# Performance work log

Hardware: AMD Instinct MI355X
Metric: run time of the kernel (lower is better)

Reference implementation:

```python
import jax, jax.numpy as jnp
import numpy as np

N_NODES = 50000
N_EDGES = 400000
IN_C, HID, EDGE_D = 128, 256, 32
NUM_LAYERS = 3

def _gnblock(x, src, dst, edge_attr, ew, eb, nw, nb):
    # edge message MLP: relu(W [x_src, x_dst, e] + b)  -> [E, HID]
    m = jax.nn.relu(jnp.concatenate([x[src], x[dst], edge_attr], axis=-1) @ ew + eb)
    # mean aggregation by destination node
    agg = jax.ops.segment_sum(m, dst, num_segments=N_NODES)
    deg = jax.ops.segment_sum(jnp.ones((m.shape[0],), m.dtype), dst, num_segments=N_NODES)
    agg = agg / jnp.maximum(deg, 1.0)[:, None]
    # node update MLP: relu(W [x, agg] + b) -> [N, HID]
    return jax.nn.relu(jnp.concatenate([x, agg], axis=-1) @ nw + nb)

def setup_inputs() -> dict:
    key = jax.random.key(0)
    ks = jax.random.split(key, 12)
    s = 0.05  # keep activations sane
    return {
        'x': jax.random.normal(ks[0], (N_NODES, IN_C), jnp.float32),
        'edge_index': jax.random.randint(ks[1], (2, N_EDGES), 0, N_NODES, jnp.int32),
        'edge_attr': jax.random.normal(ks[2], (N_EDGES, EDGE_D), jnp.float32),
        'e0_w': jax.random.normal(ks[3], (2 * IN_C + EDGE_D, HID), jnp.float32) * s,
        'e0_b': jnp.zeros((HID,), jnp.float32),
        'n0_w': jax.random.normal(ks[4], (IN_C + HID, HID), jnp.float32) * s,
        'n0_b': jnp.zeros((HID,), jnp.float32),
        'e_w': jax.random.normal(ks[5], (NUM_LAYERS - 1, 2 * HID + EDGE_D, HID), jnp.float32) * s,
        'e_b': jnp.zeros((NUM_LAYERS - 1, HID), jnp.float32),
        'n_w': jax.random.normal(ks[6], (NUM_LAYERS - 1, 2 * HID, HID), jnp.float32) * s,
        'n_b': jnp.zeros((NUM_LAYERS - 1, HID), jnp.float32),
        'h1_w': jax.random.normal(ks[7], (HID, HID), jnp.float32) * s,
        'h1_b': jnp.zeros((HID,), jnp.float32),
        'h2_w': jax.random.normal(ks[8], (HID, 1), jnp.float32) * s,
        'h2_b': jnp.zeros((1,), jnp.float32),
    }

def reference(x, edge_index, edge_attr, e0_w, e0_b, n0_w, n0_b,
              e_w, e_b, n_w, n_b, h1_w, h1_b, h2_w, h2_b):
    src, dst = edge_index[0], edge_index[1]
    h = _gnblock(x, src, dst, edge_attr, e0_w, e0_b, n0_w, n0_b)
    for i in range(NUM_LAYERS - 1):
        h = _gnblock(h, src, dst, edge_attr, e_w[i], e_b[i], n_w[i], n_b[i])
    # MLP head -> per-node logit [N, 1]
    h = jax.nn.relu(h @ h1_w + h1_b)
    return h @ h2_w + h2_b
```

## Files before the change

kernel.cpp:

```cpp
#include <hip/hip_runtime.h>
#include <hip/hip_bf16.h>
#include <hip/hip_fp16.h>

#define NN 50000
#define NE 400000
#define NBLK 196
#define PST 544

typedef unsigned short u16;
typedef unsigned int u32;
typedef __attribute__((ext_vector_type(8))) short short8;
typedef __attribute__((ext_vector_type(4))) float f32x4;
typedef __attribute__((ext_vector_type(4))) unsigned short u16x4;
typedef __attribute__((ext_vector_type(2))) _Float16 h2;
typedef __attribute__((ext_vector_type(16))) unsigned int u32x16;

typedef __attribute__((address_space(1))) const void as1_void;
typedef __attribute__((address_space(3))) void as3_void;

static __device__ __forceinline__ float bf2f(u16 u) {
    return __uint_as_float(((u32)u) << 16);
}
static __device__ __forceinline__ float bf2f_lo(u32 u) {
    return __uint_as_float(u << 16);
}
static __device__ __forceinline__ float bf2f_hi(u32 u) {
    return __uint_as_float(u & 0xffff0000u);
}
static __device__ __forceinline__ u16 f2bf(float f) {
    u32 x = __float_as_uint(f);
    x += 0x7fffu + ((x >> 16) & 1u);
    return (u16)(x >> 16);
}
static __device__ __forceinline__ u32 packbf2(float a, float b) {
    return ((u32)f2bf(b) << 16) | (u32)f2bf(a);
}
static __device__ __forceinline__ u32 packh2(float a, float b) {
    return ((u32)__half_as_ushort(__float2half(b)) << 16) |
           (u32)__half_as_ushort(__float2half(a));
}

static __device__ __forceinline__ void gload_lds16(const u16* g, u16* l) {
    __builtin_amdgcn_global_load_lds((as1_void*)g, (as3_void*)l, 16, 0, 0);
}

__global__ __launch_bounds__(256) void gemm_bt(
    const u16* __restrict__ A, int lda,
    const u16* __restrict__ Bt,
    u16* __restrict__ C, int ldc,
    int M, int K,
    const float* __restrict__ bias,
    int relu)
{
    __shared__ u16 As[128 * 32];
    __shared__ u16 Bs[128 * 32];

    const int t = threadIdx.x;
    const int w = t >> 6;
    const int lane = t & 63;
    const int quad = lane >> 4;
    const int l15 = lane & 15;
    const int tile_m = blockIdx.x * 128;
    const int tile_n = blockIdx.y * 128;
    const int wm = (w >> 1) * 64;
    const int wn = (w & 1) * 64;

    f32x4 acc[4][4];
#pragma unroll
    for (int r = 0; r < 4; ++r)
#pragma unroll
        for (int c = 0; c < 4; ++c)
            acc[r][c] = (f32x4){0.f, 0.f, 0.f, 0.f};

    int ar0 = tile_m + (t >> 2);      if (ar0 > M - 1) ar0 = M - 1;
    int ar1 = tile_m + 64 + (t >> 2); if (ar1 > M - 1) ar1 = M - 1;
    const int br0 = tile_n + (t >> 2);
    const int br1 = tile_n + 64 + (t >> 2);
    const int koff = (t & 3) * 8;

    u16* lAs0 = As + w * 512;
    u16* lAs1 = As + 2048 + w * 512;
    u16* lBs0 = Bs + w * 512;
    u16* lBs1 = Bs + 2048 + w * 512;

    const u16* Arow0 = A + (size_t)ar0 * lda + koff;
    const u16* Arow1 = A + (size_t)ar1 * lda + koff;
    const u16* Brow0 = Bt + (size_t)br0 * K + koff;
    const u16* Brow1 = Bt + (size_t)br1 * K + koff;

    for (int k0 = 0; k0 < K; k0 += 32) {
        gload_lds16(Arow0 + k0, lAs0);
        gload_lds16(Arow1 + k0, lAs1);
        gload_lds16(Brow0 + k0, lBs0);
        gload_lds16(Brow1 + k0, lBs1);
        __syncthreads();

        short8 af[4], bfr[4];
#pragma unroll
        for (int r = 0; r < 4; ++r)
            af[r] = *(const short8*)&As[(wm + r * 16 + l15) * 32 + quad * 8];
#pragma unroll
        for (int c = 0; c < 4; ++c)
            bfr[c] = *(const short8*)&Bs[(wn + c * 16 + l15) * 32 + quad * 8];
#pragma unroll
        for (int r = 0; r < 4; ++r)
#pragma unroll
            for (int c = 0; c < 4; ++c)
                acc[r][c] = __builtin_amdgcn_mfma_f32_16x16x32_bf16(af[r], bfr[c], acc[r][c], 0, 0, 0);
        __syncthreads();
    }

#pragma unroll
    for (int r = 0; r < 4; ++r) {
#pragma unroll
        for (int c = 0; c < 4; ++c) {
            const int coln = tile_n + wn + c * 16 + l15;
            const float bv = bias ? bias[coln] : 0.0f;
#pragma unroll
            for (int i = 0; i < 4; ++i) {
                const int row = tile_m + wm + r * 16 + quad * 4 + i;
                if (row < M) {
                    float v = acc[r][c][i] + bv;
                    if (relu) v = fmaxf(v, 0.f);
                    C[(size_t)row * ldc + coln] = f2bf(v);
                }
            }
        }
    }
}

__global__ __launch_bounds__(256) void edge_agg_fused(
    const u16* __restrict__ P,
    const u32* __restrict__ eattr_p32,
    const u32* __restrict__ WePk,
    const int* __restrict__ row_start,
    const int* __restrict__ src_perm,
    const float* __restrict__ inv_deg,
    u16* __restrict__ aggZ)
{
    __shared__ u32 Wlds[4096];

    const int t = threadIdx.x;
    {
        const u16* Wg = (const u16*)WePk;
        u16* Wl = (u16*)Wlds;
        const int wv = t >> 6;
        const int ln = t & 63;
#pragma unroll
        for (int r = 0; r < 4; ++r)
            gload_lds16(Wg + r * 2048 + wv * 512 + ln * 8,
                        Wl + r * 2048 + wv * 512);
    }
    __syncthreads();

    const int wid = (int)((blockIdx.x * 256 + t) >> 6);
    const int node = wid >> 1;
    const int half = wid & 1;
    const int lane = t & 63;
    const int coff = half * 128 + lane * 2;
    if (node >= NN) return;

    const u32 pdu = *(const u32*)(P + (size_t)node * PST + 256 + coff);
    const float pb0 = bf2f_lo(pdu);
    const float pb1 = bf2f_hi(pdu);

    float acc0 = 0.f, acc1 = 0.f;
    const int s0r = row_start[node], s1r = row_start[node + 1];

    if (s1r > s0r) {
        const int jlast = s1r - 1;
        const unsigned long long ebase =
            (unsigned long long)(uintptr_t)eattr_p32;

#define PSLD(ps, jj) do {                                                 \
        int js_ = __builtin_amdgcn_readfirstlane(                         \
            ((jj) < jlast) ? (jj) : jlast);                               \
        int ss_ = src_perm[js_];                                          \
        ps = *(const u32*)(P + (size_t)ss_ * PST + coff);                 \
    } while (0)

        u32 psA, psB;
        PSLD(psA, s0r);
        PSLD(psB, s0r + 1);

        for (int j = s0r; j < s1r; j += 2) {
            const u32 offA = (u32)__builtin_amdgcn_readfirstlane(j) << 6;
            const u32 offB = (u32)__builtin_amdgcn_readfirstlane(
                (j + 1 < jlast) ? j + 1 : jlast) << 6;
            u32x16 ea, eb;
            asm volatile("s_load_dwordx16 %0, %2, %3\n\t"
                         "s_load_dwordx16 %1, %2, %4"
                         : "=s"(ea), "=s"(eb)
                         : "s"(ebase), "s"(offA), "s"(offB));

            u32 psC, psD;
            PSLD(psC, j + 2);
            PSLD(psD, j + 3);

            asm volatile("s_waitcnt lgkmcnt(0)" ::: "memory");
            __builtin_amdgcn_sched_barrier(0);

            float q0A = pb0, q1A = pb1, q0B = pb0, q1B = pb1;
#define KP(idx)                                                           \
            {                                                             \
                uint2 wk = *(const uint2*)(Wlds + idx * 256 + coff);      \
                asm("v_dot2_f32_f16 %0, %4, %6, %0\n\t"                   \
                    "v_dot2_f32_f16 %1, %4, %7, %1\n\t"                   \
                    "v_dot2_f32_f16 %2, %5, %6, %2\n\t"                   \
                    "v_dot2_f32_f16 %3, %5, %7, %3"                       \
                    : "+v"(q0A), "+v"(q1A), "+v"(q0B), "+v"(q1B)          \
                    : "s"(ea[idx]), "s"(eb[idx]),                         \
                      "v"(wk.x), "v"(wk.y));                              \
            }
            KP(0)  KP(1)  KP(2)  KP(3)
            KP(4)  KP(5)  KP(6)  KP(7)
            KP(8)  KP(9)  KP(10) KP(11)
            KP(12) KP(13) KP(14) KP(15)
#undef KP

            q0A += bf2f_lo(psA);
            q1A += bf2f_hi(psA);
            acc0 += fmaxf(q0A, 0.f);
            acc1 += fmaxf(q1A, 0.f);

            q0B += bf2f_lo(psB);
            q1B += bf2f_hi(psB);
            const float m_ = (j + 1 < s1r) ? 1.0f : 0.0f;
            acc0 = fmaf(m_, fmaxf(q0B, 0.f), acc0);
            acc1 = fmaf(m_, fmaxf(q1B, 0.f), acc1);

            psA = psC;
            psB = psD;
        }
#undef PSLD
    }

    const float idg = inv_deg[node];
    *(u32*)(aggZ + (size_t)node * 512 + coff) = packbf2(acc0 * idg, acc1 * idg);
}

__global__ __launch_bounds__(256) void head_out(
    const u16* __restrict__ h4Z,
    const float* __restrict__ h2w,
    const float* __restrict__ h2b,
    float* __restrict__ out)
{
    const int node = (int)((blockIdx.x * 256 + threadIdx.x) >> 6);
    const int lane = threadIdx.x & 63;
    if (node >= NN) return;
    const int col = lane * 4;
    u16x4 hv = *(const u16x4*)(h4Z + (size_t)node * 512 + col);
    float4 wv = *(const float4*)(h2w + col);
    float s = bf2f(hv[0]) * wv.x + bf2f(hv[1]) * wv.y +
              bf2f(hv[2]) * wv.z + bf2f(hv[3]) * wv.w;
    for (int off = 32; off > 0; off >>= 1)
        s += __shfl_down(s, off, 64);
    if (lane == 0) out[node] = s + h2b[0];
}

__global__ void zero_int(int* p, int n) {
    int i = blockIdx.x * 256 + threadIdx.x;
    if (i < n) p[i] = 0;
}

__global__ void hist_k(const int* __restrict__ ei, int* __restrict__ deg) {
    int e = blockIdx.x * 256 + threadIdx.x;
    if (e < NE) atomicAdd(&deg[ei[NE + e]], 1);
}

__global__ __launch_bounds__(256) void block_sum_k(const int* __restrict__ deg,
                                                   int* __restrict__ bsum) {
    __shared__ int sm[4];
    const int i = blockIdx.x * 256 + threadIdx.x;
    int v = (i < NN) ? deg[i] : 0;
    for (int off = 32; off > 0; off >>= 1)
        v += __shfl_down(v, off, 64);
    const int lane = threadIdx.x & 63;
    const int w = threadIdx.x >> 6;
    if (lane == 0) sm[w] = v;
    __syncthreads();
    if (threadIdx.x == 0)
        bsum[blockIdx.x] = sm[0] + sm[1] + sm[2] + sm[3];
}

__global__ __launch_bounds__(256) void scan_block_k(const int* __restrict__ bsum,
                                                    int* __restrict__ boff,
                                                    int* __restrict__ row_start) {
    __shared__ int sm[256];
    const int tid = threadIdx.x;
    int v = (tid < NBLK) ? bsum[tid] : 0;
    sm[tid] = v;
    __syncthreads();
    for (int o = 1; o < 256; o <<= 1) {
        int tv = (tid >= o) ? sm[tid - o] : 0;
        __syncthreads();
        sm[tid] += tv;
        __syncthreads();
    }
    if (tid < NBLK) boff[tid] = sm[tid] - v;
    if (tid == NBLK - 1) row_start[NN] = sm[tid];
}

__global__ __launch_bounds__(256) void writeback_k(const int* __restrict__ deg,
                                                   const int* __restrict__ boff,
                                                   int* __restrict__ row_start,
                                                   int* __restrict__ cursor,
                                                   float* __restrict__ inv_deg) {
    __shared__ int sm[256];
    const int tid = threadIdx.x;
    const int i = blockIdx.x * 256 + tid;
    int v = (i < NN) ? deg[i] : 0;
    sm[tid] = v;
    __syncthreads();
    for (int o = 1; o < 256; o <<= 1) {
        int tv = (tid >= o) ? sm[tid - o] : 0;
        __syncthreads();
        sm[tid] += tv;
        __syncthreads();
    }
    if (i < NN) {
        const int rs = boff[blockIdx.x] + sm[tid] - v;
        row_start[i] = rs;
        cursor[i]    = rs;
        inv_deg[i]   = 1.0f / fmaxf((float)v, 1.0f);
    }
}

__global__ void scatter_k(const int* __restrict__ ei, const float* __restrict__ eattr,
                          int* __restrict__ cursor, int* __restrict__ src_perm,
                          u32* __restrict__ eattr_p32) {
    int e = blockIdx.x * 256 + threadIdx.x;
    if (e >= NE) return;
    int s = ei[e], d = ei[NE + e];
    int pos = atomicAdd(&cursor[d], 1);
    src_perm[pos] = s;
    const float* sr = eattr + (size_t)e * 32;
    u32 pk[16];
#pragma unroll
    for (int j = 0; j < 16; ++j)
        pk[j] = packh2(sr[2 * j], sr[2 * j + 1]);
    uint4* dr = (uint4*)(eattr_p32 + (size_t)pos * 16);
    dr[0] = (uint4){pk[0], pk[1], pk[2], pk[3]};
    dr[1] = (uint4){pk[4], pk[5], pk[6], pk[7]};
    dr[2] = (uint4){pk[8], pk[9], pk[10], pk[11]};
    dr[3] = (uint4){pk[12], pk[13], pk[14], pk[15]};
}

__global__ void bias_build(const float* __restrict__ e0b,
                           const float* __restrict__ eb1,
                           const float* __restrict__ eb2,
                           float* __restrict__ dst) {
    int i = blockIdx.x * 256 + threadIdx.x;
    if (i >= 1536) return;
    int l = i >> 9, c = i & 511;
    const float* s = (l == 0) ? e0b : (l == 1) ? eb1 : eb2;
    dst[i] = (c < 256) ? 0.f : s[c - 256];
}

struct TJob { const float* src; u16* dst; int K; int ksh; int tr; int dstride; };
struct TJobs { TJob j[16]; };

__global__ void transpose_k(TJobs jobs) {
    TJob jb = jobs.j[blockIdx.y];
    int idx = blockIdx.x * 256 + threadIdx.x;
    if (idx >= (jb.K << 8)) return;
    if (jb.tr == 1) {
        int n = idx >> jb.ksh;
        int k = idx & (jb.K - 1);
        jb.dst[n * jb.dstride + k] = f2bf(jb.src[k * 256 + n]);
    } else {
        int kp = idx >> 8;
        int c = idx & 255;
        ((u32*)jb.dst)[idx] = packh2(jb.src[(2 * kp) * 256 + c],
                                     jb.src[(2 * kp + 1) * 256 + c]);
    }
}

__global__ void cvt_x(const float* __restrict__ src, u16* __restrict__ Z) {
    int i = blockIdx.x * 256 + threadIdx.x;
    if (i >= NN * 128) return;
    int n = i >> 7, c = i & 127;
    Z[(size_t)n * 512 + 256 + c] = f2bf(src[i]);
}

extern "C" void kernel_launch(void* const* d_in, const int* in_sizes, int n_in,
                              void* d_out, int out_size, void* d_ws, size_t ws_size,
                              hipStream_t stream) {
    const float* x     = (const float*)d_in[0];
    const int*   ei    = (const int*)d_in[1];
    const float* eattr = (const float*)d_in[2];
    const float* e0_w  = (const float*)d_in[3];
    const float* e0_b  = (const float*)d_in[4];
    const float* n0_w  = (const float*)d_in[5];
    const float* n0_b  = (const float*)d_in[6];
    const float* e_w   = (const float*)d_in[7];
    const float* e_b   = (const float*)d_in[8];
    const float* n_w   = (const float*)d_in[9];
    const float* n_b   = (const float*)d_in[10];
    const float* h1_w  = (const float*)d_in[11];
    const float* h1_b  = (const float*)d_in[12];
    const float* h2_w  = (const float*)d_in[13];
    const float* h2_b  = (const float*)d_in[14];
    float* out = (float*)d_out;
    (void)in_sizes; (void)n_in; (void)out_size; (void)ws_size;

    char* base = (char*)d_ws;
    size_t off = 0;
    auto alloc = [&](size_t nbytes) -> void* {
        void* p = base + off;
        off += (nbytes + 255) & ~(size_t)255;
        return p;
    };

    int*   deg       = (int*)alloc(NN * 4);
    int*   row_start = (int*)alloc((NN + 1) * 4);
    int*   cursor    = (int*)alloc(NN * 4);
    float* invdeg    = (float*)alloc(NN * 4);
    int*   bsum      = (int*)alloc(NBLK * 4);
    int*   boff      = (int*)alloc(NBLK * 4);
    int*   src_perm  = (int*)alloc(NE * 4);
    u32*   eattr_p32 = (u32*)alloc((size_t)NE * 16 * 4);
    u16*   WcatT0    = (u16*)alloc(512 * 128 * 2);
    u16*   WcatT1    = (u16*)alloc(512 * 256 * 2);
    u16*   WcatT2    = (u16*)alloc(512 * 256 * 2);
    u32*   WePk0     = (u32*)alloc(16 * 256 * 4);
    u32*   WePk1     = (u32*)alloc(16 * 256 * 4);
    u32*   WePk2     = (u32*)alloc(16 * 256 * 4);
    u16*   BcatT0    = (u16*)alloc(256 * 384 * 2);
    u16*   BcatT1    = (u16*)alloc(256 * 512 * 2);
    u16*   BcatT2    = (u16*)alloc(256 * 512 * 2);
    u16*   H1T       = (u16*)alloc(256 * 256 * 2);
    float* bias512   = (float*)alloc(3 * 512 * 4);
    u16*   P         = (u16*)alloc((size_t)NN * PST * 2);
    u16*   Z0        = (u16*)alloc((size_t)NN * 512 * 2);
    u16*   Z1        = (u16*)alloc((size_t)NN * 512 * 2);

    zero_int<<<(NN + 255) / 256, 256, 0, stream>>>(deg, NN);
    hist_k<<<(NE + 255) / 256, 256, 0, stream>>>(ei, deg);
    block_sum_k<<<NBLK, 256, 0, stream>>>(deg, bsum);
    scan_block_k<<<1, 256, 0, stream>>>(bsum, boff, row_start);
    writeback_k<<<NBLK, 256, 0, stream>>>(deg, boff, row_start, cursor, invdeg);
    scatter_k<<<(NE + 255) / 256, 256, 0, stream>>>(ei, eattr, cursor, src_perm, eattr_p32);
    bias_build<<<6, 256, 0, stream>>>(e0_b, e_b, e_b + 256, bias512);

    const float* ew2 = e_w + 544 * 256;
    const float* nw2 = n_w + 512 * 256;

    TJobs tj;
    auto setj = [&](int i, const float* s, void* d, int K, int tr, int dstride) {
        tj.j[i].src = s; tj.j[i].dst = (u16*)d; tj.j[i].K = K; tj.j[i].tr = tr;
        tj.j[i].dstride = dstride;
        tj.j[i].ksh = (K == 256) ? 8 : (K == 128 ? 7 : 5);
    };
    setj(0,  e0_w,             WcatT0,             128, 1, 128);
    setj(1,  e0_w + 128 * 256, WcatT0 + 256 * 128, 128, 1, 128);
    setj(2,  e_w,              WcatT1,             256, 1, 256);
    setj(3,  e_w + 256 * 256,  WcatT1 + 256 * 256, 256, 1, 256);
    setj(4,  ew2,              WcatT2,             256, 1, 256);
    setj(5,  ew2 + 256 * 256,  WcatT2 + 256 * 256, 256, 1, 256);
    setj(6,  n0_w + 128 * 256, BcatT0,             256, 1, 384);
    setj(7,  n0_w,             BcatT0 + 256,       128, 1, 384);
    setj(8,  n_w + 256 * 256,  BcatT1,             256, 1, 512);
    setj(9,  n_w,              BcatT1 + 256,       256, 1, 512);
    setj(10, nw2 + 256 * 256,  BcatT2,             256, 1, 512);
    setj(11, nw2,              BcatT2 + 256,       256, 1, 512);
    setj(12, h1_w,             H1T,                256, 1, 256);
    setj(13, e0_w + 256 * 256, WePk0,              16,  2, 0);
    setj(14, e_w + 512 * 256,  WePk1,              16,  2, 0);
    setj(15, ew2 + 512 * 256,  WePk2,              16,  2, 0);
    transpose_k<<<dim3(256, 16), 256, 0, stream>>>(tj);

    cvt_x<<<(NN * 128 + 255) / 256, 256, 0, stream>>>(x, Z0);

    const int MT = (NN + 127) / 128;
    const int AGG_BLK = (2 * NN) / 4;
    u16* WcatT[3] = {WcatT0, WcatT1, WcatT2};
    u32* WePk[3]  = {WePk0, WePk1, WePk2};
    u16* BcatT[3] = {BcatT0, BcatT1, BcatT2};
    const float* nbs[3] = {n0_b, n_b, n_b + 256};
    u16* Zin[3]  = {Z0, Z1, Z0};
    u16* Zout[3] = {Z1, Z0, Z1};
    const int kin[3]   = {128, 256, 256};
    const int knode[3] = {384, 512, 512};

    for (int l = 0; l < 3; ++l) {
        gemm_bt<<<dim3(MT, 4), 256, 0, stream>>>(Zin[l] + 256, 512, WcatT[l], P, PST,
                                                 NN, kin[l], bias512 + l * 512, 0);
        edge_agg_fused<<<AGG_BLK, 256, 0, stream>>>(P, eattr_p32, WePk[l], row_start,
                                                    src_perm, invdeg, Zin[l]);
        gemm_bt<<<dim3(MT, 2), 256, 0, stream>>>(Zin[l], 512, BcatT[l], Zout[l] + 256, 512,
                                                 NN, knode[l], nbs[l], 1);
    }
    gemm_bt<<<dim3(MT, 2), 256, 0, stream>>>(Z1 + 256, 512, H1T, Z1, 512,
                                             NN, 256, h1_b, 1);
    head_out<<<NN / 4, 256, 0, stream>>>(Z1, h2_w, h2_b, out);
}
```

Before: 794.5 us.

## Process each node with one wavefront covering all 256 channels in edge aggregation

The fused edge-aggregation kernel now assigns one wavefront per destination node, each lane handling four channels, where before two wavefronts each handled half of the channels. This halves the duplicated scalar loads of edge attributes and source indices per node and widens the gathered P loads to dwordx2 with LDS weight loads of uint4. The P gather is also restructured to issue inline global loads early and wait on vmcnt only after the dot products. The cost is fewer wavefronts overall, so less parallelism for latency hiding, plus more live registers per lane.

```diff
diff --git a/kernel.cpp b/kernel.cpp
--- a/kernel.cpp
+++ b/kernel.cpp
@@ -38,6 +38,10 @@
 static __device__ __forceinline__ u32 packh2(float a, float b) {
     return ((u32)__half_as_ushort(__float2half(b)) << 16) |
            (u32)__half_as_ushort(__float2half(a));
+}
+static __device__ __forceinline__ float fdot2u(u32 a, u32 b, float c) {
+    return __builtin_amdgcn_fdot2(__builtin_bit_cast(h2, a),
+                                  __builtin_bit_cast(h2, b), c, false);
 }
 
 static __device__ __forceinline__ void gload_lds16(const u16* g, u16* l) {
@@ -153,37 +157,37 @@
     }
     __syncthreads();
 
-    const int wid = (int)((blockIdx.x * 256 + t) >> 6);
-    const int node = wid >> 1;
-    const int half = wid & 1;
+    const int node = (int)((blockIdx.x * 256 + t) >> 6);
     const int lane = t & 63;
-    const int coff = half * 128 + lane * 2;
+    const int c4 = lane * 4;
     if (node >= NN) return;
 
-    const u32 pdu = *(const u32*)(P + (size_t)node * PST + 256 + coff);
-    const float pb0 = bf2f_lo(pdu);
-    const float pb1 = bf2f_hi(pdu);
-
-    float acc0 = 0.f, acc1 = 0.f;
+    const uint2 pdu = *(const uint2*)(P + (size_t)node * PST + 256 + c4);
+    const float pb0 = bf2f_lo(pdu.x), pb1 = bf2f_hi(pdu.x);
+    const float pb2 = bf2f_lo(pdu.y), pb3 = bf2f_hi(pdu.y);
+
+    float acc0 = 0.f, acc1 = 0.f, acc2 = 0.f, acc3 = 0.f;
     const int s0r = row_start[node], s1r = row_start[node + 1];
 
     if (s1r > s0r) {
         const int jlast = s1r - 1;
         const unsigned long long ebase =
             (unsigned long long)(uintptr_t)eattr_p32;
-
-#define PSLD(ps, jj) do {                                                 \
-        int js_ = __builtin_amdgcn_readfirstlane(                         \
-            ((jj) < jlast) ? (jj) : jlast);                               \
-        int ss_ = src_perm[js_];                                          \
-        ps = *(const u32*)(P + (size_t)ss_ * PST + coff);                 \
-    } while (0)
-
-        u32 psA, psB;
-        PSLD(psA, s0r);
-        PSLD(psB, s0r + 1);
+        const u32 voff = (u32)(c4 * 2);
+
+        int ssA = src_perm[__builtin_amdgcn_readfirstlane(s0r)];
+        int ssB = src_perm[__builtin_amdgcn_readfirstlane(
+            (s0r + 1 < jlast) ? s0r + 1 : jlast)];
 
         for (int j = s0r; j < s1r; j += 2) {
+            const u16* rowpA = P + (size_t)ssA * PST;
+            const u16* rowpB = P + (size_t)ssB * PST;
+            uint2 psA, psB;
+            asm volatile("global_load_dwordx2 %0, %1, %2"
+                         : "=v"(psA) : "v"(voff), "s"(rowpA));
+            asm volatile("global_load_dwordx2 %0, %1, %2"
+                         : "=v"(psB) : "v"(voff), "s"(rowpB));
+
             const u32 offA = (u32)__builtin_amdgcn_readfirstlane(j) << 6;
             const u32 offB = (u32)__builtin_amdgcn_readfirstlane(
                 (j + 1 < jlast) ? j + 1 : jlast) << 6;
@@ -193,50 +197,52 @@
                          : "=s"(ea), "=s"(eb)
                          : "s"(ebase), "s"(offA), "s"(offB));
 
-            u32 psC, psD;
-            PSLD(psC, j + 2);
-            PSLD(psD, j + 3);
+            const int jA2 = (j + 2 < jlast) ? j + 2 : jlast;
+            const int jB2 = (j + 3 < jlast) ? j + 3 : jlast;
+            int ssA_n = src_perm[__builtin_amdgcn_readfirstlane(jA2)];
+            int ssB_n = src_perm[__builtin_amdgcn_readfirstlane(jB2)];
 
             asm volatile("s_waitcnt lgkmcnt(0)" ::: "memory");
             __builtin_amdgcn_sched_barrier(0);
 
-            float q0A = pb0, q1A = pb1, q0B = pb0, q1B = pb1;
-#define KP(idx)                                                           \
-            {                                                             \
-                uint2 wk = *(const uint2*)(Wlds + idx * 256 + coff);      \
-                asm("v_dot2_f32_f16 %0, %4, %6, %0\n\t"                   \
-                    "v_dot2_f32_f16 %1, %4, %7, %1\n\t"                   \
-                    "v_dot2_f32_f16 %2, %5, %6, %2\n\t"                   \
-                    "v_dot2_f32_f16 %3, %5, %7, %3"                       \
-                    : "+v"(q0A), "+v"(q1A), "+v"(q0B), "+v"(q1B)          \
-                    : "s"(ea[idx]), "s"(eb[idx]),                         \
-                      "v"(wk.x), "v"(wk.y));                              \
+            float qA0 = pb0, qA1 = pb1, qA2 = pb2, qA3 = pb3;
+            float qB0 = pb0, qB1 = pb1, qB2 = pb2, qB3 = pb3;
+#pragma unroll
+            for (int kp = 0; kp < 16; ++kp) {
+                uint4 wk = *(const uint4*)(Wlds + kp * 256 + c4);
+                qA0 = fdot2u(ea[kp], wk.x, qA0);
+                qA1 = fdot2u(ea[kp], wk.y, qA1);
+                qA2 = fdot2u(ea[kp], wk.z, qA2);
+                qA3 = fdot2u(ea[kp], wk.w, qA3);
+                qB0 = fdot2u(eb[kp], wk.x, qB0);
+                qB1 = fdot2u(eb[kp], wk.y, qB1);
+                qB2 = fdot2u(eb[kp], wk.z, qB2);
+                qB3 = fdot2u(eb[kp], wk.w, qB3);
             }
-            KP(0)  KP(1)  KP(2)  KP(3)
-            KP(4)  KP(5)  KP(6)  KP(7)
-            KP(8)  KP(9)  KP(10) KP(11)
-            KP(12) KP(13) KP(14) KP(15)
-#undef KP
-
-            q0A += bf2f_lo(psA);
-            q1A += bf2f_hi(psA);
-            acc0 += fmaxf(q0A, 0.f);
-            acc1 += fmaxf(q1A, 0.f);
-
-            q0B += bf2f_lo(psB);
-            q1B += bf2f_hi(psB);
-            const float m_ = (j + 1 < s1r) ? 1.0f : 0.0f;
-            acc0 = fmaf(m_, fmaxf(q0B, 0.f), acc0);
-            acc1 = fmaf(m_, fmaxf(q1B, 0.f), acc1);
-
-            psA = psC;
-            psB = psD;
+
+            asm volatile("s_waitcnt vmcnt(0)" ::: "memory");
+            __builtin_amdgcn_sched_barrier(0);
+
+            acc0 += fmaxf(qA0 + bf2f_lo(psA.x), 0.f);
+            acc1 += fmaxf(qA1 + bf2f_hi(psA.x), 0.f);
+            acc2 += fmaxf(qA2 + bf2f_lo(psA.y), 0.f);
+            acc3 += fmaxf(qA3 + bf2f_hi(psA.y), 0.f);
+            const float mB = (j + 1 < s1r) ? 1.0f : 0.0f;
+            acc0 = fmaf(mB, fmaxf(qB0 + bf2f_lo(psB.x), 0.f), acc0);
+            acc1 = fmaf(mB, fmaxf(qB1 + bf2f_hi(psB.x), 0.f), acc1);
+            acc2 = fmaf(mB, fmaxf(qB2 + bf2f_lo(psB.y), 0.f), acc2);
+            acc3 = fmaf(mB, fmaxf(qB3 + bf2f_hi(psB.y), 0.f), acc3);
+
+            ssA = ssA_n;
+            ssB = ssB_n;
         }
-#undef PSLD
     }
 
     const float idg = inv_deg[node];
-    *(u32*)(aggZ + (size_t)node * 512 + coff) = packbf2(acc0 * idg, acc1 * idg);
+    uint2 outv;
+    outv.x = packbf2(acc0 * idg, acc1 * idg);
+    outv.y = packbf2(acc2 * idg, acc3 * idg);
+    *(uint2*)(aggZ + (size_t)node * 512 + c4) = outv;
 }
 
 __global__ __launch_bounds__(256) void head_out(
@@ -473,7 +479,7 @@
     cvt_x<<<(NN * 128 + 255) / 256, 256, 0, stream>>>(x, Z0);
 
     const int MT = (NN + 127) / 128;
-    const int AGG_BLK = (2 * NN) / 4;
+    const int AGG_BLK = NN / 4;
     u16* WcatT[3] = {WcatT0, WcatT1, WcatT2};
     u32* WePk[3]  = {WePk0, WePk1, WePk2};
     u16* BcatT[3] = {BcatT0, BcatT1, BcatT2};
```

After: 754.3 us. -5.1%, faster.
